# Optimization experiments

Hardware: AMD Instinct MI355X
Metric: run time of the kernel (lower is better)

## Reference

```python
import jax, jax.numpy as jnp
import numpy as np

B, S, D = 8, 2048, 512
FF = 2048
E = 8

def setup_inputs() -> dict:
    key = jax.random.key(0)
    ks = jax.random.split(key, 7)
    s = 1.0 / np.sqrt(D)
    sf = 1.0 / np.sqrt(FF)
    return {
        "x":  jax.random.normal(ks[0], (B, S, D), dtype=jnp.float32),
        "Wg": jax.random.uniform(ks[1], (D, E), jnp.float32, -s, s),
        "bg": jax.random.uniform(ks[2], (E,), jnp.float32, -s, s),
        "W1": jax.random.uniform(ks[3], (E, D, FF), jnp.float32, -s, s),
        "b1": jax.random.uniform(ks[4], (E, FF), jnp.float32, -s, s),
        "W2": jax.random.uniform(ks[5], (E, FF, D), jnp.float32, -sf, sf),
        "b2": jax.random.uniform(ks[6], (E, D), jnp.float32, -sf, sf),
    }

def reference(x, Wg, bg, W1, b1, W2, b2):
    b, s, d = x.shape
    xf = x.reshape(-1, d)                      # [T, D]
    logits = xf @ Wg + bg                      # [T, E]
    probs = jax.nn.softmax(logits, axis=-1)
    pmax = jnp.max(probs, axis=-1)             # [T]
    routes = jnp.argmax(probs, axis=-1)        # [T] int
    xs = xf * pmax[:, None]                    # scale tokens by router prob
    # per-expert FFN over all tokens, select the routed expert's output
    out_tok = jnp.zeros_like(xf)
    for e in range(E):
        h = jax.nn.relu(xs @ W1[e] + b1[e])    # [T, FF]
        y = h @ W2[e] + b2[e]                  # [T, D]
        out_tok = jnp.where((routes == e)[:, None], y, out_tok)
    # torch.cat of per-expert nonzero-index gathers == tokens stably sorted by expert id
    order = jnp.argsort(routes)                # jnp.argsort is stable
    return out_tok[order].reshape(b, s, d)
```

## Files before the change

kernel.cpp:

```cpp
#include <hip/hip_runtime.h>
#include <hip/hip_bf16.h>

constexpr int TTOK  = 16384;
constexpr int DDIM  = 512;
constexpr int FFDIM = 2048;
constexpr int NEXP  = 8;
constexpr int GB_TOK = 16;
constexpr int NGB    = TTOK / GB_TOK;
constexpr int MAXTILES = TTOK / 128 + NEXP;

typedef __attribute__((ext_vector_type(8))) short short8_t;
typedef __attribute__((ext_vector_type(4))) float f32x4_t;

__device__ __forceinline__ unsigned short f2bf(float f) {
    union { float f; unsigned u; } v; v.f = f;
    return (unsigned short)((v.u + 0x7fffu + ((v.u >> 16) & 1u)) >> 16);
}

__device__ __forceinline__ void gl_lds16(const void* g, void* l) {
    __builtin_amdgcn_global_load_lds(
        (const __attribute__((address_space(1))) void*)g,
        (__attribute__((address_space(3))) void*)l,
        16, 0, 0);
}

__global__ __launch_bounds__(256) void transpose_cvt2(const float* __restrict__ W1,
                                                      const float* __restrict__ W2,
                                                      unsigned short* __restrict__ W1T,
                                                      unsigned short* __restrict__ W2T) {
    __shared__ float tile[32][33];
    int z = blockIdx.z;
    bool isW2 = z >= NEXP;
    int e = isW2 ? z - NEXP : z;
    int R = isW2 ? FFDIM : DDIM;
    int C = isW2 ? DDIM : FFDIM;
    int tilesC = C / 32;
    int t = blockIdx.x;
    int c0 = (t % tilesC) * 32;
    int r0 = (t / tilesC) * 32;
    const float* s = (isW2 ? W2 : W1) + (size_t)e * DDIM * FFDIM;
    unsigned short* d = (isW2 ? W2T : W1T) + (size_t)e * DDIM * FFDIM;
    int tx = threadIdx.x & 31, ty = threadIdx.x >> 5;
    #pragma unroll
    for (int i = 0; i < 4; i++)
        tile[ty + 8 * i][tx] = s[(size_t)(r0 + ty + 8 * i) * C + c0 + tx];
    __syncthreads();
    #pragma unroll
    for (int i = 0; i < 4; i++)
        d[(size_t)(c0 + ty + 8 * i) * R + r0 + tx] = f2bf(tile[tx][ty + 8 * i]);
}

__global__ __launch_bounds__(256) void gate_kernel(const float* __restrict__ x,
                                                   const float* __restrict__ Wg,
                                                   const float* __restrict__ bg,
                                                   int* __restrict__ route,
                                                   float* __restrict__ pmax,
                                                   int* __restrict__ blockCounts) {
    __shared__ int cnt[NEXP];
    __shared__ float bgs[NEXP];
    int tid = threadIdx.x;
    if (tid < NEXP) { cnt[tid] = 0; bgs[tid] = bg[tid]; }
    __syncthreads();
    int wave = tid >> 6, lane = tid & 63;
    float w[8][8];
    #pragma unroll
    for (int jj = 0; jj < 8; jj++) {
        float4 a = *(const float4*)(Wg + (size_t)(lane * 8 + jj) * NEXP);
        float4 b = *(const float4*)(Wg + (size_t)(lane * 8 + jj) * NEXP + 4);
        w[jj][0] = a.x; w[jj][1] = a.y; w[jj][2] = a.z; w[jj][3] = a.w;
        w[jj][4] = b.x; w[jj][5] = b.y; w[jj][6] = b.z; w[jj][7] = b.w;
    }
    int tbase = blockIdx.x * GB_TOK + wave * 4;
    for (int it = 0; it < 4; it++) {
        int t = tbase + it;
        float4 xa = *(const float4*)(x + (size_t)t * DDIM + lane * 8);
        float4 xb = *(const float4*)(x + (size_t)t * DDIM + lane * 8 + 4);
        float xs[8] = {xa.x, xa.y, xa.z, xa.w, xb.x, xb.y, xb.z, xb.w};
        double acc[NEXP];
        #pragma unroll
        for (int e = 0; e < NEXP; e++) acc[e] = 0.0;
        #pragma unroll
        for (int jj = 0; jj < 8; jj++) {
            double xv = (double)xs[jj];
            #pragma unroll
            for (int e = 0; e < NEXP; e++) acc[e] += xv * (double)w[jj][e];
        }
        #pragma unroll
        for (int off = 32; off > 0; off >>= 1) {
            #pragma unroll
            for (int e = 0; e < NEXP; e++) acc[e] += __shfl_down(acc[e], off);
        }
        if (lane == 0) {
            double l[NEXP];
            #pragma unroll
            for (int e = 0; e < NEXP; e++) l[e] = acc[e] + (double)bgs[e];
            int r = 0; double lm = l[0];
            #pragma unroll
            for (int e = 1; e < NEXP; e++) if (l[e] > lm) { lm = l[e]; r = e; }
            double s = 0.0;
            #pragma unroll
            for (int e = 0; e < NEXP; e++) s += exp(l[e] - lm);
            route[t] = r;
            pmax[t] = (float)(1.0 / s);
            atomicAdd(&cnt[r], 1);
        }
    }
    __syncthreads();
    if (tid < NEXP) blockCounts[blockIdx.x * NEXP + tid] = cnt[tid];
}

__global__ __launch_bounds__(1024) void scan_kernel(const int* __restrict__ blockCounts,
                                                    int* __restrict__ blockOffsets,
                                                    int* __restrict__ segPrefix,
                                                    int* __restrict__ tilePrefix) {
    __shared__ int sc[NGB][NEXP];
    __shared__ int base[NEXP + 1];
    int b = threadIdx.x;
    int c[NEXP];
    #pragma unroll
    for (int e = 0; e < NEXP; e++) { c[e] = blockCounts[b * NEXP + e]; sc[b][e] = c[e]; }
    __syncthreads();
    for (int off = 1; off < NGB; off <<= 1) {
        int t[NEXP];
        if (b >= off) {
            #pragma unroll
            for (int e = 0; e < NEXP; e++) t[e] = sc[b - off][e];
        }
        __syncthreads();
        if (b >= off) {
            #pragma unroll
            for (int e = 0; e < NEXP; e++) sc[b][e] += t[e];
        }
        __syncthreads();
    }
    if (b == 0) {
        int s = 0;
        #pragma unroll
        for (int e = 0; e < NEXP; e++) { base[e] = s; s += sc[NGB - 1][e]; }
        base[NEXP] = s;
        for (int e = 0; e <= NEXP; e++) segPrefix[e] = base[e];
        int tp = 0;
        tilePrefix[0] = 0;
        for (int e = 0; e < NEXP; e++) {
            tp += (sc[NGB - 1][e] + 127) / 128;
            tilePrefix[e + 1] = tp;
        }
    }
    __syncthreads();
    #pragma unroll
    for (int e = 0; e < NEXP; e++)
        blockOffsets[b * NEXP + e] = base[e] + sc[b][e] - c[e];
}

__global__ __launch_bounds__(256) void scatter_kernel(const float* __restrict__ x,
                                                      const int* __restrict__ route,
                                                      const float* __restrict__ pmax,
                                                      const int* __restrict__ blockOffsets,
                                                      unsigned short* __restrict__ Xs) {
    __shared__ int dstL[GB_TOK];
    __shared__ float pmL[GB_TOK];
    int tid = threadIdx.x;
    int bb = blockIdx.x;
    if (tid < GB_TOK) {
        int t = bb * GB_TOK + tid;
        int r = route[t];
        unsigned long long ltmask = (tid == 0) ? 0ull : ((~0ull) >> (64 - tid));
        int rank = 0;
        #pragma unroll
        for (int e = 0; e < NEXP; e++) {
            unsigned long long m = __ballot(r == e);
            if (r == e) rank = __popcll(m & ltmask);
        }
        dstL[tid] = blockOffsets[bb * NEXP + r] + rank;
        pmL[tid] = pmax[t];
    }
    __syncthreads();
    int wave = tid >> 6, lane = tid & 63;
    for (int rr = 0; rr < 4; rr++) {
        int rowl = wave * 4 + rr;
        int t = bb * GB_TOK + rowl;
        float pm = pmL[rowl];
        const float4* xr = (const float4*)(x + (size_t)t * DDIM) + lane * 2;
        float4 a = xr[0], b = xr[1];
        union { short8_t v; unsigned short s[8]; } o;
        o.s[0] = f2bf(a.x * pm); o.s[1] = f2bf(a.y * pm);
        o.s[2] = f2bf(a.z * pm); o.s[3] = f2bf(a.w * pm);
        o.s[4] = f2bf(b.x * pm); o.s[5] = f2bf(b.y * pm);
        o.s[6] = f2bf(b.z * pm); o.s[7] = f2bf(b.w * pm);
        *(short8_t*)(Xs + (size_t)dstL[rowl] * DDIM + lane * 8) = o.v;
    }
}

template <bool RELU, typename OutT, int K, int N>
__global__ __launch_bounds__(256) void gemm_seg(const unsigned short* __restrict__ A,
                                                const unsigned short* __restrict__ Bt,
                                                const float* __restrict__ bias,
                                                OutT* __restrict__ C,
                                                const int* __restrict__ segPrefix,
                                                const int* __restrict__ tilePrefix) {
    int t = blockIdx.x;
    if (t >= tilePrefix[NEXP]) return;
    int e = 0;
    #pragma unroll
    for (int i = 1; i <= NEXP; i++) e += (t >= tilePrefix[i]) ? 1 : 0;
    int seg1 = segPrefix[e + 1];
    int m0 = segPrefix[e] + (t - tilePrefix[e]) * 128;
    int n0 = blockIdx.y * 128;

    __shared__ unsigned short As[2 * 4096];
    __shared__ unsigned short Bs[2 * 4096];

    int tid = threadIdx.x, wave = tid >> 6, lane = tid & 63;
    const unsigned short* Bte = Bt + (size_t)e * N * K;

    int srow = lane >> 2;
    int sg   = (lane & 3) ^ ((lane >> 2) & 3) ^ ((lane >> 4) & 3);
    int scol = sg * 8;

    f32x4_t acc[4][4];
    #pragma unroll
    for (int i = 0; i < 4; i++)
        #pragma unroll
        for (int j = 0; j < 4; j++) acc[i][j] = (f32x4_t){0.f, 0.f, 0.f, 0.f};

    int wm = (wave & 1) * 64;
    int wn = (wave >> 1) * 64;
    int frow = lane & 15;
    int gr = lane >> 4;
    int fswz = (gr ^ (frow & 3) ^ ((frow >> 2) & 3)) * 8;

    int reg0 = wave * 2;
    int arow0 = m0 + reg0 * 16 + srow;
    arow0 = arow0 < TTOK ? arow0 : TTOK - 1;
    int arow1 = m0 + (reg0 + 1) * 16 + srow;
    arow1 = arow1 < TTOK ? arow1 : TTOK - 1;
    const unsigned short* aptr0 = A + (size_t)arow0 * K + scol;
    const unsigned short* aptr1 = A + (size_t)arow1 * K + scol;
    const unsigned short* bptr0 = Bte + (size_t)(n0 + reg0 * 16 + srow) * K + scol;
    const unsigned short* bptr1 = Bte + (size_t)(n0 + (reg0 + 1) * 16 + srow) * K + scol;

    #pragma unroll
    for (int kc = 0; kc < K; kc += 64) {
        #pragma unroll
        for (int p = 0; p < 2; p++) {
            gl_lds16(aptr0 + kc + p * 32, &As[p * 4096 + reg0 * 512]);
            gl_lds16(aptr1 + kc + p * 32, &As[p * 4096 + (reg0 + 1) * 512]);
            gl_lds16(bptr0 + kc + p * 32, &Bs[p * 4096 + reg0 * 512]);
            gl_lds16(bptr1 + kc + p * 32, &Bs[p * 4096 + (reg0 + 1) * 512]);
        }
        __syncthreads();
        #pragma unroll
        for (int p = 0; p < 2; p++) {
            short8_t af[4], bfr[4];
            #pragma unroll
            for (int i = 0; i < 4; i++)
                af[i] = *(const short8_t*)&As[p * 4096 + (wm + i * 16 + frow) * 32 + fswz];
            #pragma unroll
            for (int j = 0; j < 4; j++)
                bfr[j] = *(const short8_t*)&Bs[p * 4096 + (wn + j * 16 + frow) * 32 + fswz];
            #pragma unroll
            for (int i = 0; i < 4; i++)
                #pragma unroll
                for (int j = 0; j < 4; j++)
                    acc[i][j] = __builtin_amdgcn_mfma_f32_16x16x32_bf16(af[i], bfr[j], acc[i][j], 0, 0, 0);
        }
        __syncthreads();
    }

    int quad = lane >> 4;
    int colb = lane & 15;
    float bv[4];
    #pragma unroll
    for (int j = 0; j < 4; j++) bv[j] = bias[(size_t)e * N + n0 + wn + j * 16 + colb];

    if constexpr (sizeof(OutT) == 2) {
        unsigned short* cbuf = As;
        #pragma unroll
        for (int p = 0; p < 2; p++) {
            __syncthreads();
            if ((wave >> 1) == p) {
                #pragma unroll
                for (int i = 0; i < 4; i++)
                    #pragma unroll
                    for (int j = 0; j < 4; j++)
                        #pragma unroll
                        for (int r = 0; r < 4; r++) {
                            float v = acc[i][j][r] + bv[j];
                            if (RELU) v = fmaxf(v, 0.0f);
                            cbuf[(wm + i * 16 + quad * 4 + r) * 72 + j * 16 + colb] = f2bf(v);
                        }
            }
            __syncthreads();
            int row = tid >> 1, ch = (tid & 1) * 32;
            int grow = m0 + row;
            if (grow < seg1) {
                #pragma unroll
                for (int k = 0; k < 4; k++) {
                    short8_t v = *(const short8_t*)&cbuf[row * 72 + ch + k * 8];
                    *(short8_t*)&C[(size_t)grow * N + n0 + p * 64 + ch + k * 8] = v;
                }
            }
        }
    } else {
        #pragma unroll
        for (int i = 0; i < 4; i++) {
            #pragma unroll
            for (int j = 0; j < 4; j++) {
                int col = n0 + wn + j * 16 + colb;
                #pragma unroll
                for (int r = 0; r < 4; r++) {
                    int row = m0 + wm + i * 16 + quad * 4 + r;
                    if (row < seg1) {
                        float v = acc[i][j][r] + bv[j];
                        if (RELU) v = fmaxf(v, 0.0f);
                        C[(size_t)row * N + col] = v;
                    }
                }
            }
        }
    }
}

extern "C" void kernel_launch(void* const* d_in, const int* in_sizes, int n_in,
                              void* d_out, int out_size, void* d_ws, size_t ws_size,
                              hipStream_t stream) {
    const float* x  = (const float*)d_in[0];
    const float* Wg = (const float*)d_in[1];
    const float* bg = (const float*)d_in[2];
    const float* W1 = (const float*)d_in[3];
    const float* b1 = (const float*)d_in[4];
    const float* W2 = (const float*)d_in[5];
    const float* b2 = (const float*)d_in[6];
    float* out = (float*)d_out;

    char* ws = (char*)d_ws;
    size_t off = 0;
    auto alloc = [&](size_t bytes) -> char* {
        char* p = ws + off;
        off += (bytes + 255) & ~(size_t)255;
        return p;
    };
    unsigned short* W1T = (unsigned short*)alloc((size_t)NEXP * DDIM * FFDIM * 2);
    unsigned short* W2T = (unsigned short*)alloc((size_t)NEXP * DDIM * FFDIM * 2);
    unsigned short* Xs  = (unsigned short*)alloc((size_t)TTOK * DDIM * 2);
    unsigned short* H   = (unsigned short*)alloc((size_t)TTOK * FFDIM * 2);
    int*   route        = (int*)alloc((size_t)TTOK * 4);
    float* pmaxArr      = (float*)alloc((size_t)TTOK * 4);
    int*   blockCounts  = (int*)alloc((size_t)NGB * NEXP * 4);
    int*   blockOffsets = (int*)alloc((size_t)NGB * NEXP * 4);
    int*   segPrefix    = (int*)alloc((size_t)(NEXP + 1) * 4);
    int*   tilePrefix   = (int*)alloc((size_t)(NEXP + 1) * 4);

    transpose_cvt2<<<dim3(1024, 1, 2 * NEXP), 256, 0, stream>>>(W1, W2, W1T, W2T);
    gate_kernel<<<NGB, 256, 0, stream>>>(x, Wg, bg, route, pmaxArr, blockCounts);
    scan_kernel<<<1, NGB, 0, stream>>>(blockCounts, blockOffsets, segPrefix, tilePrefix);
    scatter_kernel<<<NGB, 256, 0, stream>>>(x, route, pmaxArr, blockOffsets, Xs);
    gemm_seg<true, unsigned short, DDIM, FFDIM><<<dim3(MAXTILES, FFDIM / 128, 1), 256, 0, stream>>>(
        Xs, W1T, b1, H, segPrefix, tilePrefix);
    gemm_seg<false, float, FFDIM, DDIM><<<dim3(MAXTILES, DDIM / 128, 1), 256, 0, stream>>>(
        H, W2T, b2, out, segPrefix, tilePrefix);
}
```

Baseline: 311.5 us.

## Fuse gate and weight transpose, wave-shuffle scan, swizzle tiles and epilogue LDS

Merges the weight transpose/convert kernel and the gating kernel into one launch, with blocks split by index, so the two independent jobs share a grid and one launch is dropped. The scan kernel is rewritten to use wave shuffles plus a small cross-wave pass instead of a log-step shared-memory scan with many barriers. The GEMM remaps blockIdx so consecutive blocks fall in different tile groups. It also XOR-swizzles the bf16 epilogue staging buffer to cut LDS bank conflicts. The tile remap changes cache locality and could help or hurt.

```diff
diff --git a/kernel.cpp b/kernel.cpp
--- a/kernel.cpp
+++ b/kernel.cpp
@@ -8,6 +8,8 @@
 constexpr int GB_TOK = 16;
 constexpr int NGB    = TTOK / GB_TOK;
 constexpr int MAXTILES = TTOK / 128 + NEXP;
+constexpr int PREP_GATE = NGB;
+constexpr int PREP_TR   = 16 * 1024;
 
 typedef __attribute__((ext_vector_type(8))) short short8_t;
 typedef __attribute__((ext_vector_type(4))) float f32x4_t;
@@ -24,41 +26,44 @@
         16, 0, 0);
 }
 
-__global__ __launch_bounds__(256) void transpose_cvt2(const float* __restrict__ W1,
-                                                      const float* __restrict__ W2,
-                                                      unsigned short* __restrict__ W1T,
-                                                      unsigned short* __restrict__ W2T) {
-    __shared__ float tile[32][33];
-    int z = blockIdx.z;
-    bool isW2 = z >= NEXP;
-    int e = isW2 ? z - NEXP : z;
-    int R = isW2 ? FFDIM : DDIM;
-    int C = isW2 ? DDIM : FFDIM;
-    int tilesC = C / 32;
-    int t = blockIdx.x;
-    int c0 = (t % tilesC) * 32;
-    int r0 = (t / tilesC) * 32;
-    const float* s = (isW2 ? W2 : W1) + (size_t)e * DDIM * FFDIM;
-    unsigned short* d = (isW2 ? W2T : W1T) + (size_t)e * DDIM * FFDIM;
-    int tx = threadIdx.x & 31, ty = threadIdx.x >> 5;
-    #pragma unroll
-    for (int i = 0; i < 4; i++)
-        tile[ty + 8 * i][tx] = s[(size_t)(r0 + ty + 8 * i) * C + c0 + tx];
-    __syncthreads();
-    #pragma unroll
-    for (int i = 0; i < 4; i++)
-        d[(size_t)(c0 + ty + 8 * i) * R + r0 + tx] = f2bf(tile[tx][ty + 8 * i]);
-}
-
-__global__ __launch_bounds__(256) void gate_kernel(const float* __restrict__ x,
+__global__ __launch_bounds__(256) void prep_kernel(const float* __restrict__ x,
                                                    const float* __restrict__ Wg,
                                                    const float* __restrict__ bg,
                                                    int* __restrict__ route,
                                                    float* __restrict__ pmax,
-                                                   int* __restrict__ blockCounts) {
+                                                   int* __restrict__ blockCounts,
+                                                   const float* __restrict__ W1,
+                                                   const float* __restrict__ W2,
+                                                   unsigned short* __restrict__ W1T,
+                                                   unsigned short* __restrict__ W2T) {
+    int tid = threadIdx.x;
+    if (blockIdx.x >= PREP_GATE) {
+        __shared__ float tile[32][33];
+        int id = blockIdx.x - PREP_GATE;
+        int z = id >> 10;
+        int t = id & 1023;
+        bool isW2 = z >= NEXP;
+        int e = isW2 ? z - NEXP : z;
+        int R = isW2 ? FFDIM : DDIM;
+        int C = isW2 ? DDIM : FFDIM;
+        int tilesC = C / 32;
+        int c0 = (t % tilesC) * 32;
+        int r0 = (t / tilesC) * 32;
+        const float* s = (isW2 ? W2 : W1) + (size_t)e * DDIM * FFDIM;
+        unsigned short* d = (isW2 ? W2T : W1T) + (size_t)e * DDIM * FFDIM;
+        int tx = tid & 31, ty = tid >> 5;
+        #pragma unroll
+        for (int i = 0; i < 4; i++)
+            tile[ty + 8 * i][tx] = s[(size_t)(r0 + ty + 8 * i) * C + c0 + tx];
+        __syncthreads();
+        #pragma unroll
+        for (int i = 0; i < 4; i++)
+            d[(size_t)(c0 + ty + 8 * i) * R + r0 + tx] = f2bf(tile[tx][ty + 8 * i]);
+        return;
+    }
     __shared__ int cnt[NEXP];
     __shared__ float bgs[NEXP];
-    int tid = threadIdx.x;
+    int gb = blockIdx.x;
     if (tid < NEXP) { cnt[tid] = 0; bgs[tid] = bg[tid]; }
     __syncthreads();
     int wave = tid >> 6, lane = tid & 63;
@@ -70,7 +75,7 @@
         w[jj][0] = a.x; w[jj][1] = a.y; w[jj][2] = a.z; w[jj][3] = a.w;
         w[jj][4] = b.x; w[jj][5] = b.y; w[jj][6] = b.z; w[jj][7] = b.w;
     }
-    int tbase = blockIdx.x * GB_TOK + wave * 4;
+    int tbase = gb * GB_TOK + wave * 4;
     for (int it = 0; it < 4; it++) {
         int t = tbase + it;
         float4 xa = *(const float4*)(x + (size_t)t * DDIM + lane * 8);
@@ -106,50 +111,63 @@
         }
     }
     __syncthreads();
-    if (tid < NEXP) blockCounts[blockIdx.x * NEXP + tid] = cnt[tid];
+    if (tid < NEXP) blockCounts[gb * NEXP + tid] = cnt[tid];
 }
 
 __global__ __launch_bounds__(1024) void scan_kernel(const int* __restrict__ blockCounts,
                                                     int* __restrict__ blockOffsets,
                                                     int* __restrict__ segPrefix,
                                                     int* __restrict__ tilePrefix) {
-    __shared__ int sc[NGB][NEXP];
+    int b = threadIdx.x, lane = b & 63, wv = b >> 6;
+    int c[NEXP], s[NEXP];
+    #pragma unroll
+    for (int e = 0; e < NEXP; e++) { c[e] = blockCounts[b * NEXP + e]; s[e] = c[e]; }
+    #pragma unroll
+    for (int off = 1; off < 64; off <<= 1) {
+        #pragma unroll
+        for (int e = 0; e < NEXP; e++) {
+            int t = __shfl_up(s[e], off);
+            if (lane >= off) s[e] += t;
+        }
+    }
+    __shared__ int wtot[16][NEXP];
+    __shared__ int wpre[16][NEXP];
     __shared__ int base[NEXP + 1];
-    int b = threadIdx.x;
-    int c[NEXP];
-    #pragma unroll
-    for (int e = 0; e < NEXP; e++) { c[e] = blockCounts[b * NEXP + e]; sc[b][e] = c[e]; }
-    __syncthreads();
-    for (int off = 1; off < NGB; off <<= 1) {
+    if (lane == 63) {
+        #pragma unroll
+        for (int e = 0; e < NEXP; e++) wtot[wv][e] = s[e];
+    }
+    __syncthreads();
+    if (wv == 0) {
         int t[NEXP];
-        if (b >= off) {
-            #pragma unroll
-            for (int e = 0; e < NEXP; e++) t[e] = sc[b - off][e];
-        }
-        __syncthreads();
-        if (b >= off) {
-            #pragma unroll
-            for (int e = 0; e < NEXP; e++) sc[b][e] += t[e];
-        }
-        __syncthreads();
-    }
-    if (b == 0) {
-        int s = 0;
-        #pragma unroll
-        for (int e = 0; e < NEXP; e++) { base[e] = s; s += sc[NGB - 1][e]; }
-        base[NEXP] = s;
-        for (int e = 0; e <= NEXP; e++) segPrefix[e] = base[e];
-        int tp = 0;
-        tilePrefix[0] = 0;
-        for (int e = 0; e < NEXP; e++) {
-            tp += (sc[NGB - 1][e] + 127) / 128;
-            tilePrefix[e + 1] = tp;
+        #pragma unroll
+        for (int e = 0; e < NEXP; e++) t[e] = (lane < 16) ? wtot[lane][e] : 0;
+        #pragma unroll
+        for (int off = 1; off < 16; off <<= 1) {
+            #pragma unroll
+            for (int e = 0; e < NEXP; e++) {
+                int u = __shfl_up(t[e], off);
+                if (lane >= off) t[e] += u;
+            }
+        }
+        if (lane < 16) {
+            #pragma unroll
+            for (int e = 0; e < NEXP; e++) wpre[lane][e] = t[e] - wtot[lane][e];
+        }
+        if (lane == 15) {
+            int ssum = 0;
+            #pragma unroll
+            for (int e = 0; e < NEXP; e++) { base[e] = ssum; segPrefix[e] = ssum; ssum += t[e]; }
+            base[NEXP] = ssum; segPrefix[NEXP] = ssum;
+            int tp = 0; tilePrefix[0] = 0;
+            #pragma unroll
+            for (int e = 0; e < NEXP; e++) { tp += (t[e] + 127) >> 7; tilePrefix[e + 1] = tp; }
         }
     }
     __syncthreads();
     #pragma unroll
     for (int e = 0; e < NEXP; e++)
-        blockOffsets[b * NEXP + e] = base[e] + sc[b][e] - c[e];
+        blockOffsets[b * NEXP + e] = base[e] + wpre[wv][e] + s[e] - c[e];
 }
 
 __global__ __launch_bounds__(256) void scatter_kernel(const float* __restrict__ x,
@@ -198,7 +216,9 @@
                                                 OutT* __restrict__ C,
                                                 const int* __restrict__ segPrefix,
                                                 const int* __restrict__ tilePrefix) {
-    int t = blockIdx.x;
+    int bx = blockIdx.x;
+    bx = (bx & 7) * (MAXTILES / 8) + (bx >> 3);
+    int t = bx;
     if (t >= tilePrefix[NEXP]) return;
     int e = 0;
     #pragma unroll
@@ -287,7 +307,9 @@
                         for (int r = 0; r < 4; r++) {
                             float v = acc[i][j][r] + bv[j];
                             if (RELU) v = fmaxf(v, 0.0f);
-                            cbuf[(wm + i * 16 + quad * 4 + r) * 72 + j * 16 + colb] = f2bf(v);
+                            int wrow = wm + i * 16 + quad * 4 + r;
+                            int cc = (j * 16 + colb) ^ (((wrow >> 3) & 1) * 16);
+                            cbuf[wrow * 72 + cc] = f2bf(v);
                         }
             }
             __syncthreads();
@@ -296,7 +318,8 @@
             if (grow < seg1) {
                 #pragma unroll
                 for (int k = 0; k < 4; k++) {
-                    short8_t v = *(const short8_t*)&cbuf[row * 72 + ch + k * 8];
+                    int vv = (ch + k * 8) ^ (((row >> 3) & 1) * 16);
+                    short8_t v = *(const short8_t*)&cbuf[row * 72 + vv];
                     *(short8_t*)&C[(size_t)grow * N + n0 + p * 64 + ch + k * 8] = v;
                 }
             }
@@ -351,8 +374,8 @@
     int*   segPrefix    = (int*)alloc((size_t)(NEXP + 1) * 4);
     int*   tilePrefix   = (int*)alloc((size_t)(NEXP + 1) * 4);
 
-    transpose_cvt2<<<dim3(1024, 1, 2 * NEXP), 256, 0, stream>>>(W1, W2, W1T, W2T);
-    gate_kernel<<<NGB, 256, 0, stream>>>(x, Wg, bg, route, pmaxArr, blockCounts);
+    prep_kernel<<<PREP_GATE + PREP_TR, 256, 0, stream>>>(
+        x, Wg, bg, route, pmaxArr, blockCounts, W1, W2, W1T, W2T);
     scan_kernel<<<1, NGB, 0, stream>>>(blockCounts, blockOffsets, segPrefix, tilePrefix);
     scatter_kernel<<<NGB, 256, 0, stream>>>(x, route, pmaxArr, blockOffsets, Xs);
     gemm_seg<true, unsigned short, DDIM, FFDIM><<<dim3(MAXTILES, FFDIM / 128, 1), 256, 0, stream>>>(
```

Result: no change. 311.2 us (-0.1%).
